# Kernel optimization log

Measured on AMD Instinct MI355X. Metric: run time of the kernel, lower is better.

The kernel has to match this reference:

```python
import jax, jax.numpy as jnp
import numpy as np

B, S, H, NH = 4, 2048, 1024, 16
HD = H // NH

def setup_inputs() -> dict:
    key = jax.random.key(0)
    ks = jax.random.split(key, 11)
    std = 1.0 / np.sqrt(H)
    inp = {
        'query': jax.random.normal(ks[0], (B, S, H), dtype=jnp.float32),
        'key':   jax.random.normal(ks[1], (B, S, H), dtype=jnp.float32),
        'value': jax.random.normal(ks[2], (B, S, H), dtype=jnp.float32),
        'Wq': jax.random.uniform(ks[3], (H, H), jnp.float32, -std, std),
        'bq': jax.random.uniform(ks[4], (H,), jnp.float32, -std, std),
        'Wk': jax.random.uniform(ks[5], (H, H), jnp.float32, -std, std),
        'bk': jax.random.uniform(ks[6], (H,), jnp.float32, -std, std),
        'Wv': jax.random.uniform(ks[7], (H, H), jnp.float32, -std, std),
        'bv': jax.random.uniform(ks[8], (H,), jnp.float32, -std, std),
        'Wo': jax.random.uniform(ks[9], (H, H), jnp.float32, -std, std),
        'bo': jax.random.uniform(ks[10], (H,), jnp.float32, -std, std),
    }
    return inp

def reference(query, key, value, Wq, bq, Wk, bk, Wv, bv, Wo, bo):
    def split_heads(x):  # [B,S,H] -> [B,NH,S,HD]
        return x.reshape(B, -1, NH, HD).transpose(0, 2, 1, 3)
    Q = split_heads(query @ Wq.T + bq)
    K = split_heads(key @ Wk.T + bk)
    V = split_heads(value @ Wv.T + bv)
    scores = jnp.einsum('bhqd,bhkd->bhqk', Q, K) / np.sqrt(HD).astype(np.float32)
    weights = jax.nn.softmax(scores, axis=-1)
    attn = jnp.einsum('bhqk,bhkd->bhqd', weights, V)  # [B,NH,S,HD]
    attn = attn.transpose(0, 2, 1, 3).reshape(B, -1, H)
    return attn @ Wo.T + bo
```

## Files before the change

kernel.cpp:

```cpp
#include <hip/hip_runtime.h>
#include <hip/hip_bf16.h>

typedef __attribute__((ext_vector_type(4)))  float f32x4;
typedef __attribute__((ext_vector_type(16))) float f32x16;
typedef __attribute__((ext_vector_type(8)))  short bf16x8;
typedef __attribute__((ext_vector_type(4)))  short bf16x4;

#define DEVI static __device__ __forceinline__

constexpr int Bn = 4, Sn = 2048, Hn = 1024, NHn = 16, HDn = 64;
constexpr int Kn = 1024, Nn = 1024;
constexpr float QSCALE = 0.18033688011112042f;

DEVI unsigned short f2bf(float x) {
    union { float f; unsigned u; } v; v.f = x;
    unsigned r = v.u + 0x7fffu + ((v.u >> 16) & 1u);
    return (unsigned short)(r >> 16);
}

DEVI f32x4 mfma16(bf16x8 a, bf16x8 b, f32x4 c) {
    return __builtin_amdgcn_mfma_f32_16x16x32_bf16(a, b, c, 0, 0, 0);
}
DEVI f32x16 mfma32(bf16x8 a, bf16x8 b, f32x16 c) {
    return __builtin_amdgcn_mfma_f32_32x32x16_bf16(a, b, c, 0, 0, 0);
}
DEVI unsigned cvt_pk_bf16(float lo, float hi) {
    unsigned r;
    asm("v_cvt_pk_bf16_f32 %0, %1, %2" : "=v"(r) : "v"(lo), "v"(hi));
    return r;
}
DEVI void pl32swap(unsigned &a, unsigned &b) {
    asm("v_permlane32_swap_b32 %0, %1" : "+v"(a), "+v"(b));
}
DEVI float exp2_raw(float x) { return __builtin_amdgcn_exp2f(x); }

typedef const __attribute__((address_space(1))) void* gas1_t;
typedef __attribute__((address_space(3))) void* gas3_t;

__global__ void convert_w_kernel(const float* __restrict__ w0, const float* __restrict__ w1,
                                 const float* __restrict__ w2, const float* __restrict__ w3,
                                 unsigned short* __restrict__ out)
{
    int mat = blockIdx.x >> 10;
    int i4  = ((blockIdx.x & 1023) << 8) + threadIdx.x;
    const float* w = mat == 0 ? w0 : mat == 1 ? w1 : mat == 2 ? w2 : w3;
    f32x4 v = *reinterpret_cast<const f32x4*>(w + (size_t)i4 * 4);
    union { unsigned u[2]; bf16x4 s; } pk;
    pk.u[0] = cvt_pk_bf16(v[0], v[1]);
    pk.u[1] = cvt_pk_bf16(v[2], v[3]);
    *reinterpret_cast<bf16x4*>(out + (((size_t)mat) << 20) + (size_t)i4 * 4) = pk.s;
}

__global__ __launch_bounds__(256, 2)
void out_proj_kernel(const unsigned short* __restrict__ Aw, const unsigned short* __restrict__ Bw,
                     const float* __restrict__ bias, float* __restrict__ Out)
{
    __shared__ __align__(16) unsigned short As[128 * 32];
    __shared__ __align__(16) unsigned short Bs[128 * 32];

    const int tid = threadIdx.x;
    const int wid = tid >> 6, lane = tid & 63;
    const int lhi = lane >> 4, llo = lane & 15;
    const int bid = blockIdx.x;
    const int sid = (bid & 7) * 64 + (bid >> 3);
    const int bx = sid & 7, by = sid >> 3;
    const int brow = by * 128, bcol = bx * 128;
    const int wr = wid >> 1, wc = wid & 1;

    f32x4 acc[4][4] = {};

    for (int kt = 0; kt < Kn / 32; ++kt) {
        __syncthreads();
        #pragma unroll
        for (int r = 0; r < 2; ++r) {
            int lin = r * 256 + tid;
            int row = lin >> 2, kc = (lin & 3) * 8;
            __builtin_amdgcn_global_load_lds(
                (gas1_t)(Bw + (size_t)(bcol + row) * Kn + kt * 32 + kc),
                (gas3_t)(Bs + (size_t)(r * 256 + wid * 64) * 8), 16, 0, 0);
        }
        #pragma unroll
        for (int r = 0; r < 2; ++r) {
            int lin = r * 256 + tid;
            int row = lin >> 2, kc = (lin & 3) * 8;
            __builtin_amdgcn_global_load_lds(
                (gas1_t)(Aw + (size_t)(brow + row) * Kn + kt * 32 + kc),
                (gas3_t)(As + (size_t)(r * 256 + wid * 64) * 8), 16, 0, 0);
        }
        __syncthreads();

        bf16x8 a[4], b[4];
        #pragma unroll
        for (int m = 0; m < 4; ++m)
            a[m] = *reinterpret_cast<const bf16x8*>(As + (wr * 64 + m * 16 + llo) * 32 + lhi * 8);
        #pragma unroll
        for (int n = 0; n < 4; ++n)
            b[n] = *reinterpret_cast<const bf16x8*>(Bs + (wc * 64 + n * 16 + llo) * 32 + lhi * 8);
        #pragma unroll
        for (int m = 0; m < 4; ++m)
            #pragma unroll
            for (int n = 0; n < 4; ++n)
                acc[m][n] = mfma16(a[m], b[n], acc[m][n]);
    }

    #pragma unroll
    for (int m = 0; m < 4; ++m)
        #pragma unroll
        for (int n = 0; n < 4; ++n) {
            const int col  = bcol + wc * 64 + n * 16 + llo;
            const int row0 = brow + wr * 64 + m * 16 + lhi * 4;
            const float bv = bias[col];
            #pragma unroll
            for (int r = 0; r < 4; ++r)
                Out[(size_t)(row0 + r) * Nn + col] = acc[m][n][r] + bv;
        }
}

__global__ __launch_bounds__(256, 2)
void qkv_proj_kernel(const float* __restrict__ xq, const float* __restrict__ xk,
                     const float* __restrict__ xv, const unsigned short* __restrict__ Wb,
                     const float* __restrict__ bq, const float* __restrict__ bk,
                     const float* __restrict__ bv,
                     unsigned short* __restrict__ Qw, unsigned short* __restrict__ Kw,
                     unsigned short* __restrict__ Vw)
{
    __shared__ __align__(16) unsigned short As[2][128 * 32];
    __shared__ __align__(16) unsigned short Bs[2][128 * 32];

    const int z = blockIdx.z;
    const float* A           = z == 0 ? xq : z == 1 ? xk : xv;
    const unsigned short* W  = Wb + (((size_t)z) << 20);
    const float* bias        = z == 0 ? bq : z == 1 ? bk : bv;
    unsigned short* Out      = z == 0 ? Qw : z == 1 ? Kw : Vw;
    const float scale        = z == 0 ? QSCALE : 1.0f;

    const int tid = threadIdx.x;
    const int wid = tid >> 6, lane = tid & 63;
    const int lhi = lane >> 4, llo = lane & 15;
    const int bid = blockIdx.x;
    const int sid = (bid & 7) * 64 + (bid >> 3);
    const int bx = sid & 7, by = sid >> 3;
    const int brow = by * 128, bcol = bx * 128;
    const int wr = wid >> 1, wc = wid & 1;

    f32x4 acc[4][4] = {};

    auto issueA = [&](f32x4 (&ar)[4], int kt) {
        #pragma unroll
        for (int r = 0; r < 4; ++r) {
            int lin = r * 256 + tid;
            int row = lin >> 3, kc = (lin & 7) * 4;
            ar[r] = *reinterpret_cast<const f32x4*>(A + (size_t)(brow + row) * Kn + kt * 32 + kc);
        }
    };
    auto stageB = [&](int buf, int kt) {
        #pragma unroll
        for (int r = 0; r < 2; ++r) {
            int lin = r * 256 + tid;
            int row = lin >> 2, kc = (lin & 3) * 8;
            __builtin_amdgcn_global_load_lds(
                (gas1_t)(W + (size_t)(bcol + row) * Kn + kt * 32 + kc),
                (gas3_t)(Bs[buf] + (size_t)(r * 256 + wid * 64) * 8), 16, 0, 0);
        }
    };
    auto writeA = [&](int buf, f32x4 (&ar)[4]) {
        #pragma unroll
        for (int r = 0; r < 4; ++r) {
            int lin = r * 256 + tid;
            int row = lin >> 3, kc = (lin & 7) * 4;
            union { unsigned u[2]; bf16x4 s; } pk;
            pk.u[0] = cvt_pk_bf16(ar[r][0], ar[r][1]);
            pk.u[1] = cvt_pk_bf16(ar[r][2], ar[r][3]);
            *reinterpret_cast<bf16x4*>(As[buf] + row * 32 + kc) = pk.s;
        }
    };
    auto compute = [&](int buf) {
        bf16x8 a[4], b[4];
        #pragma unroll
        for (int m = 0; m < 4; ++m)
            a[m] = *reinterpret_cast<const bf16x8*>(As[buf] + (wr * 64 + m * 16 + llo) * 32 + lhi * 8);
        #pragma unroll
        for (int n = 0; n < 4; ++n)
            b[n] = *reinterpret_cast<const bf16x8*>(Bs[buf] + (wc * 64 + n * 16 + llo) * 32 + lhi * 8);
        #pragma unroll
        for (int m = 0; m < 4; ++m)
            #pragma unroll
            for (int n = 0; n < 4; ++n)
                acc[m][n] = mfma16(a[m], b[n], acc[m][n]);
    };

    constexpr int NKT = Kn / 32;
    f32x4 ar0[4], ar1[4];

    issueA(ar0, 0);
    stageB(0, 0);
    writeA(0, ar0);
    __syncthreads();

    for (int kt = 0; kt < NKT; kt += 2) {
        issueA(ar1, kt + 1);
        stageB(1, kt + 1);
        compute(0);
        writeA(1, ar1);
        __syncthreads();
        if (kt + 2 < NKT) { issueA(ar0, kt + 2); stageB(0, kt + 2); }
        compute(1);
        if (kt + 2 < NKT) writeA(0, ar0);
        __syncthreads();
    }

    #pragma unroll
    for (int m = 0; m < 4; ++m) {
        #pragma unroll
        for (int n = 0; n < 4; ++n) {
            const int col  = bcol + wc * 64 + n * 16 + llo;
            const int row0 = brow + wr * 64 + m * 16 + lhi * 4;
            const float bv = bias[col];
            const int hh = col >> 6, d = col & 63;
            if (z != 2) {
                unsigned short* O = (unsigned short*)Out;
                #pragma unroll
                for (int r = 0; r < 4; ++r) {
                    int rowm = row0 + r;
                    int bb = rowm >> 11, ss = rowm & 2047;
                    O[((((size_t)bb * NHn + hh) * Sn + ss) << 6) + d] =
                        f2bf((acc[m][n][r] + bv) * scale);
                }
            } else {
                unsigned short* O = (unsigned short*)Out;
                const int bb = row0 >> 11, ss = row0 & 2047;
                union { unsigned u[2]; bf16x4 s; } pk;
                pk.u[0] = cvt_pk_bf16(acc[m][n][0] + bv, acc[m][n][1] + bv);
                pk.u[1] = cvt_pk_bf16(acc[m][n][2] + bv, acc[m][n][3] + bv);
                *reinterpret_cast<bf16x4*>(O + (((size_t)bb * NHn + hh) * HDn + d) * Sn + ss) = pk.s;
            }
        }
    }
}

__global__ __launch_bounds__(256, 2)
void attn_kernel(const unsigned short* __restrict__ Q, const unsigned short* __restrict__ K,
                 const unsigned short* __restrict__ Vt, unsigned short* __restrict__ On)
{
    __shared__ __align__(16) unsigned short LDST[2 * 2 * 4096];

    const int tid = threadIdx.x;
    const int wid = tid >> 6, lane = tid & 63;
    const int l31 = lane & 31, h = lane >> 5;
    const int bid = blockIdx.x;
    const int sid = (bid & 7) * 64 + (bid >> 3);
    const int bh = sid >> 3;
    const int qt = sid & 7;
    const int q0 = qt * 256 + wid * 64;

    const unsigned short* Qb = Q + (size_t)bh * Sn * HDn;
    const unsigned short* Kb = K + (size_t)bh * Sn * HDn;
    const unsigned short* Vb = Vt + (size_t)bh * HDn * Sn;

    int koff[2], voff[2];
    #pragma unroll
    for (int r = 0; r < 2; ++r) {
        int lin = (r * 256 + tid) * 16;
        int row = lin >> 7, colb = lin & 127;
        int scolb = colb ^ ((row & 7) << 4);
        koff[r] = row * HDn + (scolb >> 1);
        voff[r] = row * Sn + (scolb >> 1);
    }

    auto stage = [&](int buf, int key0) {
        #pragma unroll
        for (int r = 0; r < 2; ++r)
            __builtin_amdgcn_global_load_lds((gas1_t)(Kb + koff[r] + key0 * HDn),
                (gas3_t)(LDST + buf * 8192 + r * 2048 + wid * 512), 16, 0, 0);
        #pragma unroll
        for (int r = 0; r < 2; ++r)
            __builtin_amdgcn_global_load_lds((gas1_t)(Vb + voff[r] + key0),
                (gas3_t)(LDST + buf * 8192 + 4096 + r * 2048 + wid * 512), 16, 0, 0);
    };

    auto rdT = [&](int byteoff) -> bf16x8 {
        return *reinterpret_cast<const bf16x8*>((const char*)LDST + byteoff);
    };
    const int lrow = l31 * 128;
    const int lswz = (l31 & 7) << 4;

    bf16x8 qfA[4], qfB[4];
    #pragma unroll
    for (int sd = 0; sd < 4; ++sd) {
        qfA[sd] = *reinterpret_cast<const bf16x8*>(Qb + (size_t)(q0 + l31) * HDn + sd * 16 + h * 8);
        qfB[sd] = *reinterpret_cast<const bf16x8*>(Qb + (size_t)(q0 + 32 + l31) * HDn + sd * 16 + h * 8);
    }

    f32x16 oA0 = {}, oA1 = {}, oB0 = {}, oB1 = {};
    float lA = 0.f, lB = 0.f;

    stage(0, 0);
    __syncthreads();

    auto body = [&](int buf) {
        const int base = buf * 16384;
        bf16x8 ka0[4], ka1[4];
        #pragma unroll
        for (int sd = 0; sd < 4; ++sd) {
            int la = lrow + ((sd * 32 + h * 16) ^ lswz);
            ka0[sd] = rdT(base + la);
            ka1[sd] = rdT(base + 4096 + la);
        }
        f32x16 sA0 = {}, sA1 = {}, sB0 = {}, sB1 = {};
        __builtin_amdgcn_s_setprio(1);
        #pragma unroll
        for (int sd = 0; sd < 4; ++sd) sA0 = mfma32(ka0[sd], qfA[sd], sA0);
        #pragma unroll
        for (int sd = 0; sd < 4; ++sd) sA1 = mfma32(ka1[sd], qfA[sd], sA1);
        #pragma unroll
        for (int sd = 0; sd < 4; ++sd) sB0 = mfma32(ka0[sd], qfB[sd], sB0);
        #pragma unroll
        for (int sd = 0; sd < 4; ++sd) sB1 = mfma32(ka1[sd], qfB[sd], sB1);
        __builtin_amdgcn_s_setprio(0);

        bf16x8 va0[4], va1[4];
        #pragma unroll
        for (int S = 0; S < 4; ++S) {
            int la = lrow + ((S * 32 + h * 16) ^ lswz);
            va0[S] = rdT(base + 8192 + la);
            va1[S] = rdT(base + 8192 + 4096 + la);
        }

        #pragma unroll
        for (int r = 0; r < 16; ++r) {
            sA0[r] = exp2_raw(sA0[r]); sA1[r] = exp2_raw(sA1[r]);
            sB0[r] = exp2_raw(sB0[r]); sB1[r] = exp2_raw(sB1[r]);
        }

        {
            float sa[16], sb[16];
            #pragma unroll
            for (int r = 0; r < 16; ++r) { sa[r] = sA0[r] + sA1[r]; sb[r] = sB0[r] + sB1[r]; }
            #pragma unroll
            for (int st = 8; st > 0; st >>= 1)
                #pragma unroll
                for (int r = 0; r < 8; ++r)
                    if (r < st) { sa[r] += sa[r + st]; sb[r] += sb[r + st]; }
            lA += sa[0];
            lB += sb[0];
        }

        unsigned WpA[2][4][2], WpB[2][4][2];
        #pragma unroll
        for (int R = 0; R < 4; ++R) {
            WpA[0][R][0] = cvt_pk_bf16(sA0[4 * R],     sA0[4 * R + 1]);
            WpA[0][R][1] = cvt_pk_bf16(sA0[4 * R + 2], sA0[4 * R + 3]);
            WpA[1][R][0] = cvt_pk_bf16(sA1[4 * R],     sA1[4 * R + 1]);
            WpA[1][R][1] = cvt_pk_bf16(sA1[4 * R + 2], sA1[4 * R + 3]);
            WpB[0][R][0] = cvt_pk_bf16(sB0[4 * R],     sB0[4 * R + 1]);
            WpB[0][R][1] = cvt_pk_bf16(sB0[4 * R + 2], sB0[4 * R + 3]);
            WpB[1][R][0] = cvt_pk_bf16(sB1[4 * R],     sB1[4 * R + 1]);
            WpB[1][R][1] = cvt_pk_bf16(sB1[4 * R + 2], sB1[4 * R + 3]);
        }

        #pragma unroll
        for (int kc = 0; kc < 2; ++kc) {
            #pragma unroll
            for (int sp = 0; sp < 2; ++sp) {
                const int S = kc * 2 + sp;
                unsigned a0 = WpA[kc][2 * sp][0], a2 = WpA[kc][2 * sp + 1][0];
                unsigned a1 = WpA[kc][2 * sp][1], a3 = WpA[kc][2 * sp + 1][1];
                pl32swap(a0, a2);
                pl32swap(a1, a3);
                union { unsigned u[4]; bf16x8 v; } pbA;
                pbA.u[0] = a0; pbA.u[1] = a1; pbA.u[2] = a2; pbA.u[3] = a3;
                unsigned b0 = WpB[kc][2 * sp][0], b2 = WpB[kc][2 * sp + 1][0];
                unsigned b1 = WpB[kc][2 * sp][1], b3 = WpB[kc][2 * sp + 1][1];
                pl32swap(b0, b2);
                pl32swap(b1, b3);
                union { unsigned u[4]; bf16x8 v; } pbB;
                pbB.u[0] = b0; pbB.u[1] = b1; pbB.u[2] = b2; pbB.u[3] = b3;
                __builtin_amdgcn_s_setprio(1);
                oA0 = mfma32(va0[S], pbA.v, oA0);
                oA1 = mfma32(va1[S], pbA.v, oA1);
                oB0 = mfma32(va0[S], pbB.v, oB0);
                oB1 = mfma32(va1[S], pbB.v, oB1);
                __builtin_amdgcn_s_setprio(0);
            }
        }
    };

    constexpr int NT = Sn / 64;
    for (int kt = 0; kt < NT; kt += 2) {
        stage(1, (kt + 1) * 64);
        body(0);
        __syncthreads();
        if (kt + 2 < NT) stage(0, (kt + 2) * 64);
        body(1);
        __syncthreads();
    }

    lA += __shfl_xor(lA, 32, 64);
    lB += __shfl_xor(lB, 32, 64);
    const float invA = 1.f / lA, invB = 1.f / lB;
    const int b = bh >> 4, hh = bh & 15;
    unsigned short* OrowA = On + ((size_t)b * Sn + (q0 + l31))      * Hn + hh * 64;
    unsigned short* OrowB = On + ((size_t)b * Sn + (q0 + 32 + l31)) * Hn + hh * 64;
    #pragma unroll
    for (int g = 0; g < 4; ++g) {
        union { unsigned u[2]; bf16x4 s; } pA0, pA1, pB0, pB1;
        pA0.u[0] = cvt_pk_bf16(oA0[4 * g] * invA,     oA0[4 * g + 1] * invA);
        pA0.u[1] = cvt_pk_bf16(oA0[4 * g + 2] * invA, oA0[4 * g + 3] * invA);
        pA1.u[0] = cvt_pk_bf16(oA1[4 * g] * invA,     oA1[4 * g + 1] * invA);
        pA1.u[1] = cvt_pk_bf16(oA1[4 * g + 2] * invA, oA1[4 * g + 3] * invA);
        pB0.u[0] = cvt_pk_bf16(oB0[4 * g] * invB,     oB0[4 * g + 1] * invB);
        pB0.u[1] = cvt_pk_bf16(oB0[4 * g + 2] * invB, oB0[4 * g + 3] * invB);
        pB1.u[0] = cvt_pk_bf16(oB1[4 * g] * invB,     oB1[4 * g + 1] * invB);
        pB1.u[1] = cvt_pk_bf16(oB1[4 * g + 2] * invB, oB1[4 * g + 3] * invB);
        *reinterpret_cast<bf16x4*>(OrowA + g * 8 + 4 * h)      = pA0.s;
        *reinterpret_cast<bf16x4*>(OrowA + 32 + g * 8 + 4 * h) = pA1.s;
        *reinterpret_cast<bf16x4*>(OrowB + g * 8 + 4 * h)      = pB0.s;
        *reinterpret_cast<bf16x4*>(OrowB + 32 + g * 8 + 4 * h) = pB1.s;
    }
}

extern "C" void kernel_launch(void* const* d_in, const int* in_sizes, int n_in,
                              void* d_out, int out_size, void* d_ws, size_t ws_size,
                              hipStream_t stream)
{
    (void)in_sizes; (void)n_in; (void)out_size;
    const float* q  = (const float*)d_in[0];
    const float* k  = (const float*)d_in[1];
    const float* v  = (const float*)d_in[2];
    const float* Wq = (const float*)d_in[3];
    const float* bq = (const float*)d_in[4];
    const float* Wk = (const float*)d_in[5];
    const float* bk = (const float*)d_in[6];
    const float* Wv = (const float*)d_in[7];
    const float* bv = (const float*)d_in[8];
    const float* Wo = (const float*)d_in[9];
    const float* bo = (const float*)d_in[10];
    float* out = (float*)d_out;

    if (ws_size < (size_t)72 * 1024 * 1024) return;

    unsigned short* Wb = (unsigned short*)d_ws;
    unsigned short* Qw = Wb + (size_t)4 * 1024 * 1024;
    unsigned short* Kw = Qw + (size_t)8 * 1024 * 1024;
    unsigned short* Vw = Kw + (size_t)8 * 1024 * 1024;
    unsigned short* Aw = Vw + (size_t)8 * 1024 * 1024;

    convert_w_kernel<<<4096, 256, 0, stream>>>(Wq, Wk, Wv, Wo, Wb);
    qkv_proj_kernel<<<dim3(512, 1, 3), 256, 0, stream>>>(q, k, v, Wb, bq, bk, bv, Qw, Kw, Vw);
    attn_kernel<<<512, 256, 0, stream>>>(Qw, Kw, Vw, Aw);
    out_proj_kernel<<<512, 256, 0, stream>>>(Aw, Wb + ((size_t)3 << 20), bo, out);
}
```

Before: 185.5 us.

## Triple-buffer LDS staging with vmcnt waits and single barrier in all GEMM/attention loops

```diff
diff --git a/kernel.cpp b/kernel.cpp
--- a/kernel.cpp
+++ b/kernel.cpp
@@ -7,6 +7,10 @@
 typedef __attribute__((ext_vector_type(4)))  short bf16x4;
 
 #define DEVI static __device__ __forceinline__
+#define WAITV(N) asm volatile("s_waitcnt vmcnt(" #N ")" ::: "memory")
+#define WAITLGKM0 asm volatile("s_waitcnt lgkmcnt(0)" ::: "memory")
+#define BAR() __builtin_amdgcn_s_barrier()
+#define SCHEDB() __builtin_amdgcn_sched_barrier(0)
 
 constexpr int Bn = 4, Sn = 2048, Hn = 1024, NHn = 16, HDn = 64;
 constexpr int Kn = 1024, Nn = 1024;
@@ -17,7 +21,6 @@
     unsigned r = v.u + 0x7fffu + ((v.u >> 16) & 1u);
     return (unsigned short)(r >> 16);
 }
-
 DEVI f32x4 mfma16(bf16x8 a, bf16x8 b, f32x4 c) {
     return __builtin_amdgcn_mfma_f32_16x16x32_bf16(a, b, c, 0, 0, 0);
 }
@@ -51,12 +54,12 @@
     *reinterpret_cast<bf16x4*>(out + (((size_t)mat) << 20) + (size_t)i4 * 4) = pk.s;
 }
 
-__global__ __launch_bounds__(256, 2)
+__global__ __launch_bounds__(256, 3)
 void out_proj_kernel(const unsigned short* __restrict__ Aw, const unsigned short* __restrict__ Bw,
                      const float* __restrict__ bias, float* __restrict__ Out)
 {
-    __shared__ __align__(16) unsigned short As[128 * 32];
-    __shared__ __align__(16) unsigned short Bs[128 * 32];
+    __shared__ __align__(16) unsigned short As[3][128 * 32];
+    __shared__ __align__(16) unsigned short Bs[3][128 * 32];
 
     const int tid = threadIdx.x;
     const int wid = tid >> 6, lane = tid & 63;
@@ -69,15 +72,14 @@
 
     f32x4 acc[4][4] = {};
 
-    for (int kt = 0; kt < Kn / 32; ++kt) {
-        __syncthreads();
+    auto stage = [&](unsigned short* as, unsigned short* bs, int kt) {
         #pragma unroll
         for (int r = 0; r < 2; ++r) {
             int lin = r * 256 + tid;
             int row = lin >> 2, kc = (lin & 3) * 8;
             __builtin_amdgcn_global_load_lds(
                 (gas1_t)(Bw + (size_t)(bcol + row) * Kn + kt * 32 + kc),
-                (gas3_t)(Bs + (size_t)(r * 256 + wid * 64) * 8), 16, 0, 0);
+                (gas3_t)(bs + (size_t)(r * 256 + wid * 64) * 8), 16, 0, 0);
         }
         #pragma unroll
         for (int r = 0; r < 2; ++r) {
@@ -85,22 +87,37 @@
             int row = lin >> 2, kc = (lin & 3) * 8;
             __builtin_amdgcn_global_load_lds(
                 (gas1_t)(Aw + (size_t)(brow + row) * Kn + kt * 32 + kc),
-                (gas3_t)(As + (size_t)(r * 256 + wid * 64) * 8), 16, 0, 0);
-        }
-        __syncthreads();
-
+                (gas3_t)(as + (size_t)(r * 256 + wid * 64) * 8), 16, 0, 0);
+        }
+    };
+    auto compute = [&](const unsigned short* as, const unsigned short* bs) {
         bf16x8 a[4], b[4];
         #pragma unroll
         for (int m = 0; m < 4; ++m)
-            a[m] = *reinterpret_cast<const bf16x8*>(As + (wr * 64 + m * 16 + llo) * 32 + lhi * 8);
+            a[m] = *reinterpret_cast<const bf16x8*>(as + (wr * 64 + m * 16 + llo) * 32 + lhi * 8);
         #pragma unroll
         for (int n = 0; n < 4; ++n)
-            b[n] = *reinterpret_cast<const bf16x8*>(Bs + (wc * 64 + n * 16 + llo) * 32 + lhi * 8);
+            b[n] = *reinterpret_cast<const bf16x8*>(bs + (wc * 64 + n * 16 + llo) * 32 + lhi * 8);
         #pragma unroll
         for (int m = 0; m < 4; ++m)
             #pragma unroll
             for (int n = 0; n < 4; ++n)
                 acc[m][n] = mfma16(a[m], b[n], acc[m][n]);
+    };
+
+    stage(As[0], Bs[0], 0);
+    int bc = 0, bn = 1, b2 = 2;
+    constexpr int NKT = Kn / 32;
+    for (int n = 0; n < NKT; ++n) {
+        if (n + 1 < NKT) {
+            stage(As[bn], Bs[bn], n + 1);
+            WAITV(4);
+        } else {
+            WAITV(0);
+        }
+        BAR(); SCHEDB();
+        compute(As[bc], Bs[bc]);
+        int t = bc; bc = bn; bn = b2; b2 = t;
     }
 
     #pragma unroll
@@ -116,7 +133,7 @@
         }
 }
 
-__global__ __launch_bounds__(256, 2)
+__global__ __launch_bounds__(256, 4)
 void qkv_proj_kernel(const float* __restrict__ xq, const float* __restrict__ xk,
                      const float* __restrict__ xv, const unsigned short* __restrict__ Wb,
                      const float* __restrict__ bq, const float* __restrict__ bk,
@@ -125,7 +142,7 @@
                      unsigned short* __restrict__ Vw)
 {
     __shared__ __align__(16) unsigned short As[2][128 * 32];
-    __shared__ __align__(16) unsigned short Bs[2][128 * 32];
+    __shared__ __align__(16) unsigned short Bs[3][128 * 32];
 
     const int z = blockIdx.z;
     const float* A           = z == 0 ? xq : z == 1 ? xk : xv;
@@ -144,8 +161,9 @@
     const int wr = wid >> 1, wc = wid & 1;
 
     f32x4 acc[4][4] = {};
-
-    auto issueA = [&](f32x4 (&ar)[4], int kt) {
+    f32x4 ar[4];
+
+    auto issueA = [&](int kt) {
         #pragma unroll
         for (int r = 0; r < 4; ++r) {
             int lin = r * 256 + tid;
@@ -153,17 +171,17 @@
             ar[r] = *reinterpret_cast<const f32x4*>(A + (size_t)(brow + row) * Kn + kt * 32 + kc);
         }
     };
-    auto stageB = [&](int buf, int kt) {
+    auto stageB = [&](unsigned short* bs, int kt) {
         #pragma unroll
         for (int r = 0; r < 2; ++r) {
             int lin = r * 256 + tid;
             int row = lin >> 2, kc = (lin & 3) * 8;
             __builtin_amdgcn_global_load_lds(
                 (gas1_t)(W + (size_t)(bcol + row) * Kn + kt * 32 + kc),
-                (gas3_t)(Bs[buf] + (size_t)(r * 256 + wid * 64) * 8), 16, 0, 0);
-        }
-    };
-    auto writeA = [&](int buf, f32x4 (&ar)[4]) {
+                (gas3_t)(bs + (size_t)(r * 256 + wid * 64) * 8), 16, 0, 0);
+        }
+    };
+    auto writeA = [&](unsigned short* as) {
         #pragma unroll
         for (int r = 0; r < 4; ++r) {
             int lin = r * 256 + tid;
@@ -171,17 +189,17 @@
             union { unsigned u[2]; bf16x4 s; } pk;
             pk.u[0] = cvt_pk_bf16(ar[r][0], ar[r][1]);
             pk.u[1] = cvt_pk_bf16(ar[r][2], ar[r][3]);
-            *reinterpret_cast<bf16x4*>(As[buf] + row * 32 + kc) = pk.s;
-        }
-    };
-    auto compute = [&](int buf) {
+            *reinterpret_cast<bf16x4*>(as + row * 32 + kc) = pk.s;
+        }
+    };
+    auto compute = [&](const unsigned short* as, const unsigned short* bs) {
         bf16x8 a[4], b[4];
         #pragma unroll
         for (int m = 0; m < 4; ++m)
-            a[m] = *reinterpret_cast<const bf16x8*>(As[buf] + (wr * 64 + m * 16 + llo) * 32 + lhi * 8);
+            a[m] = *reinterpret_cast<const bf16x8*>(as + (wr * 64 + m * 16 + llo) * 32 + lhi * 8);
         #pragma unroll
         for (int n = 0; n < 4; ++n)
-            b[n] = *reinterpret_cast<const bf16x8*>(Bs[buf] + (wc * 64 + n * 16 + llo) * 32 + lhi * 8);
+            b[n] = *reinterpret_cast<const bf16x8*>(bs + (wc * 64 + n * 16 + llo) * 32 + lhi * 8);
         #pragma unroll
         for (int m = 0; m < 4; ++m)
             #pragma unroll
@@ -190,23 +208,23 @@
     };
 
     constexpr int NKT = Kn / 32;
-    f32x4 ar0[4], ar1[4];
-
-    issueA(ar0, 0);
-    stageB(0, 0);
-    writeA(0, ar0);
-    __syncthreads();
-
-    for (int kt = 0; kt < NKT; kt += 2) {
-        issueA(ar1, kt + 1);
-        stageB(1, kt + 1);
-        compute(0);
-        writeA(1, ar1);
-        __syncthreads();
-        if (kt + 2 < NKT) { issueA(ar0, kt + 2); stageB(0, kt + 2); }
-        compute(1);
-        if (kt + 2 < NKT) writeA(0, ar0);
-        __syncthreads();
+    issueA(0);
+    stageB(Bs[0], 0);
+    writeA(As[0]);
+    int bc = 0, bn = 1, b2 = 2;
+    for (int n = 0; n < NKT; ++n) {
+        if (n + 1 < NKT) {
+            issueA(n + 1);
+            stageB(Bs[bn], n + 1);
+            WAITV(6);
+        } else {
+            WAITV(0);
+        }
+        WAITLGKM0;
+        BAR(); SCHEDB();
+        compute(As[n & 1], Bs[bc]);
+        if (n + 1 < NKT) writeA(As[(n + 1) & 1]);
+        int t = bc; bc = bn; bn = b2; b2 = t;
     }
 
     #pragma unroll
@@ -238,11 +256,11 @@
     }
 }
 
-__global__ __launch_bounds__(256, 2)
+__global__ __launch_bounds__(256, 3)
 void attn_kernel(const unsigned short* __restrict__ Q, const unsigned short* __restrict__ K,
                  const unsigned short* __restrict__ Vt, unsigned short* __restrict__ On)
 {
-    __shared__ __align__(16) unsigned short LDST[2 * 2 * 4096];
+    __shared__ __align__(16) unsigned short LDST[3 * 8192];
 
     const int tid = threadIdx.x;
     const int wid = tid >> 6, lane = tid & 63;
@@ -267,17 +285,16 @@
         voff[r] = row * Sn + (scolb >> 1);
     }
 
-    auto stage = [&](int buf, int key0) {
+    auto stage = [&](int bufEl, int key0) {
         #pragma unroll
         for (int r = 0; r < 2; ++r)
             __builtin_amdgcn_global_load_lds((gas1_t)(Kb + koff[r] + key0 * HDn),
-                (gas3_t)(LDST + buf * 8192 + r * 2048 + wid * 512), 16, 0, 0);
+                (gas3_t)(LDST + bufEl + r * 2048 + wid * 512), 16, 0, 0);
         #pragma unroll
         for (int r = 0; r < 2; ++r)
             __builtin_amdgcn_global_load_lds((gas1_t)(Vb + voff[r] + key0),
-                (gas3_t)(LDST + buf * 8192 + 4096 + r * 2048 + wid * 512), 16, 0, 0);
-    };
-
+                (gas3_t)(LDST + bufEl + 4096 + r * 2048 + wid * 512), 16, 0, 0);
+    };
     auto rdT = [&](int byteoff) -> bf16x8 {
         return *reinterpret_cast<const bf16x8*>((const char*)LDST + byteoff);
     };
@@ -294,11 +311,7 @@
     f32x16 oA0 = {}, oA1 = {}, oB0 = {}, oB1 = {};
     float lA = 0.f, lB = 0.f;
 
-    stage(0, 0);
-    __syncthreads();
-
-    auto body = [&](int buf) {
-        const int base = buf * 16384;
+    auto body = [&](int base) {
         bf16x8 ka0[4], ka1[4];
         #pragma unroll
         for (int sd = 0; sd < 4; ++sd) {
@@ -386,13 +399,18 @@
     };
 
     constexpr int NT = Sn / 64;
-    for (int kt = 0; kt < NT; kt += 2) {
-        stage(1, (kt + 1) * 64);
-        body(0);
-        __syncthreads();
-        if (kt + 2 < NT) stage(0, (kt + 2) * 64);
-        body(1);
-        __syncthreads();
+    stage(0, 0);
+    int ec = 0, en = 8192, e2 = 16384;
+    for (int n = 0; n < NT; ++n) {
+        if (n + 1 < NT) {
+            stage(en, (n + 1) * 64);
+            WAITV(4);
+        } else {
+            WAITV(0);
+        }
+        BAR(); SCHEDB();
+        body(ec * 2);
+        int t = ec; ec = en; en = e2; e2 = t;
     }
 
     lA += __shfl_xor(lA, 32, 64);
```

After: 494.1 us. 166% more time.

## Triple-buffer K/V LDS staging with vmcnt waits and a single barrier

Applied to the files above, without the earlier changes.

```diff
diff --git a/kernel.cpp b/kernel.cpp
--- a/kernel.cpp
+++ b/kernel.cpp
@@ -7,6 +7,9 @@
 typedef __attribute__((ext_vector_type(4)))  short bf16x4;
 
 #define DEVI static __device__ __forceinline__
+#define WAITV(N) asm volatile("s_waitcnt vmcnt(" #N ")" ::: "memory")
+#define BAR() __builtin_amdgcn_s_barrier()
+#define SCHEDB() __builtin_amdgcn_sched_barrier(0)
 
 constexpr int Bn = 4, Sn = 2048, Hn = 1024, NHn = 16, HDn = 64;
 constexpr int Kn = 1024, Nn = 1024;
@@ -242,7 +245,7 @@
 void attn_kernel(const unsigned short* __restrict__ Q, const unsigned short* __restrict__ K,
                  const unsigned short* __restrict__ Vt, unsigned short* __restrict__ On)
 {
-    __shared__ __align__(16) unsigned short LDST[2 * 2 * 4096];
+    __shared__ __align__(16) unsigned short LDST[3 * 8192];
 
     const int tid = threadIdx.x;
     const int wid = tid >> 6, lane = tid & 63;
@@ -267,17 +270,16 @@
         voff[r] = row * Sn + (scolb >> 1);
     }
 
-    auto stage = [&](int buf, int key0) {
+    auto stage = [&](int bufEl, int key0) {
         #pragma unroll
         for (int r = 0; r < 2; ++r)
             __builtin_amdgcn_global_load_lds((gas1_t)(Kb + koff[r] + key0 * HDn),
-                (gas3_t)(LDST + buf * 8192 + r * 2048 + wid * 512), 16, 0, 0);
+                (gas3_t)(LDST + bufEl + r * 2048 + wid * 512), 16, 0, 0);
         #pragma unroll
         for (int r = 0; r < 2; ++r)
             __builtin_amdgcn_global_load_lds((gas1_t)(Vb + voff[r] + key0),
-                (gas3_t)(LDST + buf * 8192 + 4096 + r * 2048 + wid * 512), 16, 0, 0);
-    };
-
+                (gas3_t)(LDST + bufEl + 4096 + r * 2048 + wid * 512), 16, 0, 0);
+    };
     auto rdT = [&](int byteoff) -> bf16x8 {
         return *reinterpret_cast<const bf16x8*>((const char*)LDST + byteoff);
     };
@@ -294,11 +296,7 @@
     f32x16 oA0 = {}, oA1 = {}, oB0 = {}, oB1 = {};
     float lA = 0.f, lB = 0.f;
 
-    stage(0, 0);
-    __syncthreads();
-
-    auto body = [&](int buf) {
-        const int base = buf * 16384;
+    auto body = [&](int base) {
         bf16x8 ka0[4], ka1[4];
         #pragma unroll
         for (int sd = 0; sd < 4; ++sd) {
@@ -386,13 +384,18 @@
     };
 
     constexpr int NT = Sn / 64;
-    for (int kt = 0; kt < NT; kt += 2) {
-        stage(1, (kt + 1) * 64);
-        body(0);
-        __syncthreads();
-        if (kt + 2 < NT) stage(0, (kt + 2) * 64);
-        body(1);
-        __syncthreads();
+    stage(0, 0);
+    int ec = 0, en = 8192, e2 = 16384;
+    for (int n = 0; n < NT; ++n) {
+        if (n + 1 < NT) {
+            stage(en, (n + 1) * 64);
+            WAITV(4);
+        } else {
+            WAITV(0);
+        }
+        BAR(); SCHEDB();
+        body(ec * 2);
+        int t = ec; ec = en; en = e2; e2 = t;
     }
 
     lA += __shfl_xor(lA, 32, 64);
```

After: 186.2 us. About the same (+0.3%).
